# Kernel optimization log

Measured on AMD Instinct MI355X. Metric: run time of the kernel, lower is better.

## Reference

```python
import jax, jax.numpy as jnp
import numpy as np

B, T, E, A = 8, 2048, 1024, 1024


def setup_inputs() -> dict:
    key = jax.random.key(0)
    k1, k2, k3, k4 = jax.random.split(key, 4)
    embedded = jax.random.normal(k1, (B, T, E), dtype=jnp.float32)
    s = 1.0 / np.sqrt(E)
    # nn.Linear(E, A, bias=False) stores weight of shape (A, E); y = x @ W^T
    Wq = jax.random.uniform(k2, (A, E), dtype=jnp.float32, minval=-s, maxval=s)
    Wk = jax.random.uniform(k3, (A, E), dtype=jnp.float32, minval=-s, maxval=s)
    Wv = jax.random.uniform(k4, (A, E), dtype=jnp.float32, minval=-s, maxval=s)
    return {"embedded": embedded, "Wq": Wq, "Wk": Wk, "Wv": Wv}


def reference(embedded, Wq, Wk, Wv):
    # q, k, v: [B, T, A]
    q = jnp.einsum("bte,ae->bta", embedded, Wq)
    k = jnp.einsum("bte,ae->bta", embedded, Wk)
    v = jnp.einsum("bte,ae->bta", embedded, Wv)
    scale = 1.0 / jnp.sqrt(jnp.asarray(Wq.shape[0], dtype=q.dtype))
    # causal scores: [B, T, T]
    scores = jnp.einsum("bqa,bka->bqk", q, k) * scale
    t = scores.shape[-1]
    causal = jnp.tril(jnp.ones((t, t), dtype=bool))
    scores = jnp.where(causal, scores, jnp.asarray(-jnp.inf, dtype=scores.dtype))
    attn = jax.nn.softmax(scores, axis=-1)
    return jnp.einsum("bqk,bka->bqa", attn, v)
```

## Files before the change

### kernel.cpp

```cpp
#include <hip/hip_runtime.h>
#include <hip/hip_bf16.h>
#include <stdint.h>


#define BB 8
#define TT 2048
#define EE 1024
#define AA 1024
#define MM (BB * TT)

typedef short bf16x8 __attribute__((ext_vector_type(8)));
typedef float f32x4 __attribute__((ext_vector_type(4)));

#define GLOAD_LDS16(g, l)                                                      \
  __builtin_amdgcn_global_load_lds(                                            \
      (const __attribute__((address_space(1))) void*)(g),                      \
      (__attribute__((address_space(3))) void*)(l), 16, 0, 0)

#define SBAR()                               \
  do {                                       \
    __builtin_amdgcn_sched_barrier(0);       \
    __builtin_amdgcn_s_barrier();            \
    __builtin_amdgcn_sched_barrier(0);       \
  } while (0)

#define LGKM(n)                                               \
  do {                                                        \
    asm volatile("s_waitcnt lgkmcnt(" #n ")" ::: "memory");   \
    __builtin_amdgcn_sched_barrier(0);                        \
  } while (0)

#define VMCNT(n)                                              \
  do {                                                        \
    asm volatile("s_waitcnt vmcnt(" #n ")" ::: "memory");     \
    __builtin_amdgcn_sched_barrier(0);                        \
  } while (0)

#define MFMA16(a, b, c) __builtin_amdgcn_mfma_f32_16x16x32_bf16((a), (b), (c), 0, 0, 0)

__device__ __forceinline__ void gemm256_core(
    const short* __restrict__ gA, int lda, int a0row,
    const short* __restrict__ gB, int ldb, int b0row, int NT, short* As,
    short* Bs, f32x4 (*acc)[4]) {
  const int tid = threadIdx.x;
  const int lane = tid & 63;
  const int w = tid >> 6;
  const int lrow = lane & 15;
  const int lk8 = (lane >> 4) * 8;
  const int swz = ((lrow >> 3) & 1) << 4;
  const int wr = w >> 2, wc = w & 3;
  const int baseA = (((wr * 128 + lrow) * 32) + lk8) ^ swz;
  const int baseB = (((wc * 64 + lrow) * 32) + lk8) ^ swz;

  const short* pA[2];
  const short* pB[2];
#pragma unroll
  for (int i = 0; i < 2; ++i) {
    int chunk = 2 * w + i;
    int P = chunk * 1024 + lane * 16;
    int L = P ^ (((P >> 9) & 1) << 5);
    int row = L >> 6;
    int kb2 = (L & 63) >> 1;
    pA[i] = gA + (size_t)(a0row + row) * lda + kb2;
    pB[i] = gB + (size_t)(b0row + row) * ldb + kb2;
  }

#define STG_A(tl, s)                                                           \
  do {                                                                         \
    int _o = (tl) * 64 + (s) * 32;                                             \
    short* _d = As + (((tl) & 1) << 14) + ((s) << 13);                         \
    GLOAD_LDS16(pA[0] + _o, _d + (2 * w) * 512 + lane * 8);                    \
    GLOAD_LDS16(pA[1] + _o, _d + (2 * w + 1) * 512 + lane * 8);                \
  } while (0)
#define STG_B(tl, s)                                                           \
  do {                                                                         \
    int _o = (tl) * 64 + (s) * 32;                                             \
    short* _d = Bs + (((tl) & 1) << 14) + ((s) << 13);                         \
    GLOAD_LDS16(pB[0] + _o, _d + (2 * w) * 512 + lane * 8);                    \
    GLOAD_LDS16(pB[1] + _o, _d + (2 * w + 1) * 512 + lane * 8);                \
  } while (0)

  STG_B(0, 0); STG_A(0, 0); STG_B(0, 1); STG_A(0, 1);
  bf16x8 a0[4], b0[4];
  if (NT > 1) {
    STG_B(1, 0); STG_A(1, 0); STG_B(1, 1);
    VMCNT(6);
  } else {
    VMCNT(0);
  }
  SBAR();
#pragma unroll
  for (int m = 0; m < 4; ++m) a0[m] = *(const bf16x8*)&As[baseA + m * 512];
#pragma unroll
  for (int n = 0; n < 4; ++n) b0[n] = *(const bf16x8*)&Bs[baseB + n * 512];

  for (int t = 0; t < NT; ++t) {
    const short* Ac = As + ((t & 1) << 14);
    const short* Bc = Bs + ((t & 1) << 14);
    const short* An = As + (((t + 1) & 1) << 14);
    const short* Bn = Bs + (((t + 1) & 1) << 14);
    bf16x8 a1[4], a2[4], a3[4], b1[4];

    if (t < NT - 1) {
      STG_A(t + 1, 1);
      VMCNT(8);
    } else {
      VMCNT(0);
    }
    SBAR();
#pragma unroll
    for (int m = 0; m < 4; ++m)
      a1[m] = *(const bf16x8*)&Ac[baseA + (m + 4) * 512];
#pragma unroll
    for (int m = 0; m < 4; ++m)
      a2[m] = *(const bf16x8*)&Ac[8192 + baseA + m * 512];
    LGKM(8);
    __builtin_amdgcn_s_setprio(1);
#pragma unroll
    for (int m = 0; m < 4; ++m)
#pragma unroll
      for (int n = 0; n < 4; ++n) acc[m][n] = MFMA16(a0[m], b0[n], acc[m][n]);
    __builtin_amdgcn_s_setprio(0);
    SBAR();

    if (t < NT - 2) STG_B(t + 2, 0);
    SBAR();
#pragma unroll
    for (int n = 0; n < 4; ++n)
      b1[n] = *(const bf16x8*)&Bc[8192 + baseB + n * 512];
    LGKM(4);
    __builtin_amdgcn_s_setprio(1);
#pragma unroll
    for (int m = 0; m < 4; ++m)
#pragma unroll
      for (int n = 0; n < 4; ++n)
        acc[m + 4][n] = MFMA16(a1[m], b0[n], acc[m + 4][n]);
    __builtin_amdgcn_s_setprio(0);
    SBAR();

    if (t < NT - 2) STG_A(t + 2, 0);
    SBAR();
#pragma unroll
    for (int m = 0; m < 4; ++m)
      a3[m] = *(const bf16x8*)&Ac[8192 + baseA + (m + 4) * 512];
    LGKM(4);
    __builtin_amdgcn_s_setprio(1);
#pragma unroll
    for (int m = 0; m < 4; ++m)
#pragma unroll
      for (int n = 0; n < 4; ++n) acc[m][n] = MFMA16(a2[m], b1[n], acc[m][n]);
    __builtin_amdgcn_s_setprio(0);
    SBAR();

    if (t < NT - 2) {
      STG_B(t + 2, 1);
      VMCNT(10);
    } else if (t == NT - 2) {
      VMCNT(4);
    }
    SBAR();
    if (t < NT - 1) {
#pragma unroll
      for (int m = 0; m < 4; ++m) a0[m] = *(const bf16x8*)&An[baseA + m * 512];
#pragma unroll
      for (int n = 0; n < 4; ++n) b0[n] = *(const bf16x8*)&Bn[baseB + n * 512];
      LGKM(8);
    } else {
      LGKM(0);
    }
    __builtin_amdgcn_s_setprio(1);
#pragma unroll
    for (int m = 0; m < 4; ++m)
#pragma unroll
      for (int n = 0; n < 4; ++n)
        acc[m + 4][n] = MFMA16(a3[m], b1[n], acc[m + 4][n]);
    __builtin_amdgcn_s_setprio(0);
    SBAR();
  }
#undef STG_A
#undef STG_B
}

__global__ __launch_bounds__(512, 2) void qkv_gemm8(
    const short* __restrict__ xb, const short* __restrict__ Wb,
    short* __restrict__ qkv) {
  __shared__ __align__(16) short As[32768];
  __shared__ __align__(16) short Bs[32768];
  int f = blockIdx.x;
  int s = (f & 7) * 96 + (f >> 3);
  int mt = s / 12, nt = s % 12;
  int z = nt >> 2, ntl = nt & 3;
  const short* gB = Wb + (size_t)z * AA * EE + (size_t)(ntl * 256) * EE;
  f32x4 acc[8][4];
#pragma unroll
  for (int m = 0; m < 8; ++m)
#pragma unroll
    for (int n = 0; n < 4; ++n) acc[m][n] = (f32x4){0.f, 0.f, 0.f, 0.f};
  gemm256_core(xb, EE, mt * 256, gB, EE, 0, EE / 64, As, Bs, acc);

  short* o = qkv + (size_t)z * MM * AA;
  int lane = threadIdx.x & 63, w = threadIdx.x >> 6, wr = w >> 2, wc = w & 3;
  int lrow = lane & 15, lk4 = (lane >> 4) * 4;
  int row0 = mt * 256 + wr * 128;
  int col0 = ntl * 256 + wc * 64;
#pragma unroll
  for (int m = 0; m < 8; ++m)
#pragma unroll
    for (int n = 0; n < 4; ++n)
#pragma unroll
      for (int r = 0; r < 4; ++r) {
        int row = row0 + m * 16 + lk4 + r;
        int col = col0 + n * 16 + lrow;
        __hip_bfloat16 h = __float2bfloat16(acc[m][n][r]);
        o[(size_t)row * AA + col] = *(short*)&h;
      }
}

__device__ __forceinline__ void stage_tile(const short* __restrict__ g,
                                           size_t stride, short* lds, int tid) {
#pragma unroll
  for (int r = 0; r < 4; ++r) {
    int t = r * 256 + tid;
    int row = t >> 3;
    int c = (t & 7) * 8;
    GLOAD_LDS16(g + (size_t)row * stride + c, lds + (size_t)t * 8);
  }
}

__device__ __forceinline__ void mfma_step(const short* As, const short* Bs,
                                          f32x4 acc[4][4], int lane, int wr,
                                          int wc) {
  int lrow = lane & 15;
  int lk = (lane >> 4) * 8;
#pragma unroll
  for (int kk = 0; kk < 64; kk += 32) {
    bf16x8 a[4], b[4];
#pragma unroll
    for (int i = 0; i < 4; ++i)
      a[i] = *(const bf16x8*)&As[(wr * 64 + i * 16 + lrow) * 64 + kk + lk];
#pragma unroll
    for (int j = 0; j < 4; ++j)
      b[j] = *(const bf16x8*)&Bs[(wc * 64 + j * 16 + lrow) * 64 + kk + lk];
#pragma unroll
    for (int i = 0; i < 4; ++i)
#pragma unroll
      for (int j = 0; j < 4; ++j)
        acc[i][j] =
            __builtin_amdgcn_mfma_f32_16x16x32_bf16(a[i], b[j], acc[i][j], 0, 0, 0);
  }
}

__global__ void cvt_bf16(const float* __restrict__ src, short* __restrict__ dst,
                         int n4) {
  int stride = gridDim.x * blockDim.x;
  for (int i = blockIdx.x * blockDim.x + threadIdx.x; i < n4; i += stride) {
    float4 v = ((const float4*)src)[i];
    __hip_bfloat16 h0 = __float2bfloat16(v.x);
    __hip_bfloat16 h1 = __float2bfloat16(v.y);
    __hip_bfloat16 h2 = __float2bfloat16(v.z);
    __hip_bfloat16 h3 = __float2bfloat16(v.w);
    short4 o;
    o.x = *(short*)&h0;
    o.y = *(short*)&h1;
    o.z = *(short*)&h2;
    o.w = *(short*)&h3;
    ((short4*)dst)[i] = o;
  }
}

__global__ void cvt_w3(const float* __restrict__ wq, const float* __restrict__ wk,
                       const float* __restrict__ wv, short* __restrict__ dst) {
  const int n4 = AA * EE / 4;
  int stride = gridDim.x * blockDim.x;
  for (int i = blockIdx.x * blockDim.x + threadIdx.x; i < 3 * n4; i += stride) {
    const float* src = (i < n4) ? wq : (i < 2 * n4 ? wk : wv);
    int ii = (i < n4) ? i : (i < 2 * n4 ? i - n4 : i - 2 * n4);
    float4 v = ((const float4*)src)[ii];
    __hip_bfloat16 h0 = __float2bfloat16(v.x);
    __hip_bfloat16 h1 = __float2bfloat16(v.y);
    __hip_bfloat16 h2 = __float2bfloat16(v.z);
    __hip_bfloat16 h3 = __float2bfloat16(v.w);
    short4 o;
    o.x = *(short*)&h0;
    o.y = *(short*)&h1;
    o.z = *(short*)&h2;
    o.w = *(short*)&h3;
    ((short4*)dst)[i] = o;
  }
}

__global__ __launch_bounds__(256) void transpose_v(const short* __restrict__ Vb,
                                                   short* __restrict__ Vt) {
  __shared__ __align__(16) short lds[64 * 72];
  int t0 = blockIdx.x * 64;
  int d0 = blockIdx.y * 64;
  int b = blockIdx.z;
  int tid = threadIdx.x;
  const short* src = Vb + ((size_t)b * TT + t0) * AA + d0;
#pragma unroll
  for (int r = 0; r < 2; ++r) {
    int t = r * 256 + tid;
    int row = t >> 3;
    int c = (t & 7) * 8;
    *(bf16x8*)&lds[row * 72 + c] = *(const bf16x8*)&src[(size_t)row * AA + c];
  }
  __syncthreads();
  short* dst = Vt + ((size_t)b * AA + d0) * TT + t0;
#pragma unroll
  for (int r = 0; r < 2; ++r) {
    int t = r * 256 + tid;
    int d = t >> 3;
    int c = (t & 7) * 8;
    bf16x8 wv;
#pragma unroll
    for (int e = 0; e < 8; ++e) wv[e] = lds[(c + e) * 72 + d];
    *(bf16x8*)&dst[(size_t)d * TT + c] = wv;
  }
}

__global__ __launch_bounds__(256) void score_gemm(const short* __restrict__ Qb,
                                                  const short* __restrict__ Kb,
                                                  short* __restrict__ Pu,
                                                  float* __restrict__ lsum) {
  int f = blockIdx.x;
  int b = f & 7;
  int j = f >> 3;
  int mt = 0;
  while ((mt + 1) * (mt + 2) / 2 <= j) ++mt;
  int nt = j - mt * (mt + 1) / 2;
  int q0 = mt * 128, c0 = nt * 128;

  __shared__ __align__(16) short As[128 * 64];
  __shared__ __align__(16) short Bs[128 * 64];
  int tid = threadIdx.x;
  int lane = tid & 63, wid = tid >> 6, wr = wid >> 1, wc = wid & 1;
  const short* Q = Qb + (size_t)b * TT * AA;
  const short* K = Kb + (size_t)b * TT * AA;
  f32x4 acc[4][4];
#pragma unroll
  for (int i = 0; i < 4; ++i)
#pragma unroll
    for (int jj = 0; jj < 4; ++jj) acc[i][jj] = (f32x4){0.f, 0.f, 0.f, 0.f};

  for (int k0 = 0; k0 < AA; k0 += 64) {
    stage_tile(Q + (size_t)q0 * AA + k0, AA, As, tid);
    stage_tile(K + (size_t)c0 * AA + k0, AA, Bs, tid);
    __syncthreads();
    mfma_step(As, Bs, acc, lane, wr, wc);
    __syncthreads();
  }
  const float scale = 0.03125f;
  short* P = Pu + (size_t)b * TT * TT;
  int lrow = lane & 15, lk4 = (lane >> 4) * 4;
#pragma unroll
  for (int i = 0; i < 4; ++i) {
#pragma unroll
    for (int r = 0; r < 4; ++r) {
      int q = q0 + wr * 64 + i * 16 + lk4 + r;
      float rs = 0.f;
#pragma unroll
      for (int jj = 0; jj < 4; ++jj) {
        int kx = c0 + wc * 64 + jj * 16 + lrow;
        float e = (kx <= q) ? __expf(acc[i][jj][r] * scale) : 0.f;
        rs += e;
        __hip_bfloat16 h = __float2bfloat16(e);
        P[(size_t)q * TT + kx] = *(short*)&h;
      }
      rs += __shfl_xor(rs, 1);
      rs += __shfl_xor(rs, 2);
      rs += __shfl_xor(rs, 4);
      rs += __shfl_xor(rs, 8);
      if (lrow == 0) atomicAdd(&lsum[b * TT + q], rs);
    }
  }
}

__global__ __launch_bounds__(256) void pv_gemm(const short* __restrict__ Pu,
                                               const short* __restrict__ Vt,
                                               const float* __restrict__ lsum,
                                               float* __restrict__ out) {
  int f = blockIdx.x;
  int b = f & 7;
  int j = f >> 3;
  int p = j >> 3;
  int nt = j & 7;
  int n0 = nt * 128;

  __shared__ __align__(16) short As[128 * 64];
  __shared__ __align__(16) short Bs[128 * 64];
  int tid = threadIdx.x;
  int lane = tid & 63, wid = tid >> 6, wr = wid >> 1, wc = wid & 1;
  const short* P = Pu + (size_t)b * TT * TT;
  const short* V = Vt + (size_t)b * AA * TT;
  int lrow = lane & 15, lk4 = (lane >> 4) * 4;

#pragma unroll
  for (int s = 0; s < 2; ++s) {
    int mt = s ? (15 - p) : p;
    int q0 = mt * 128;
    f32x4 acc[4][4];
#pragma unroll
    for (int i = 0; i < 4; ++i)
#pragma unroll
      for (int jj = 0; jj < 4; ++jj) acc[i][jj] = (f32x4){0.f, 0.f, 0.f, 0.f};

    int kend = q0 + 128;
    for (int k0 = 0; k0 < kend; k0 += 64) {
      stage_tile(P + (size_t)q0 * TT + k0, TT, As, tid);
      stage_tile(V + (size_t)n0 * TT + k0, TT, Bs, tid);
      __syncthreads();
      mfma_step(As, Bs, acc, lane, wr, wc);
      __syncthreads();
    }
#pragma unroll
    for (int i = 0; i < 4; ++i) {
#pragma unroll
      for (int r = 0; r < 4; ++r) {
        int q = q0 + wr * 64 + i * 16 + lk4 + r;
        float linv = 1.0f / lsum[b * TT + q];
#pragma unroll
        for (int jj = 0; jj < 4; ++jj) {
          int d = n0 + wc * 64 + jj * 16 + lrow;
          out[((size_t)(b * TT + q)) * AA + d] = acc[i][jj][r] * linv;
        }
      }
    }
  }
}

extern "C" void kernel_launch(void* const* d_in, const int* in_sizes, int n_in,
                              void* d_out, int out_size, void* d_ws,
                              size_t ws_size, hipStream_t stream) {
  const float* x = (const float*)d_in[0];
  const float* Wq = (const float*)d_in[1];
  const float* Wk = (const float*)d_in[2];
  const float* Wv = (const float*)d_in[3];

  char* ws = (char*)d_ws;
  size_t oWb = 0;
  size_t oQb = oWb + (size_t)3 * AA * EE * 2;
  size_t oKb = oQb + (size_t)MM * AA * 2;
  size_t oVb = oKb + (size_t)MM * AA * 2;
  size_t oVt = oVb + (size_t)MM * AA * 2;
  size_t oLs = oVt + (size_t)MM * AA * 2;
  size_t oXb = oLs + (size_t)MM * 4;
  size_t oPu = oXb;

  short* Wb = (short*)(ws + oWb);
  short* Qb = (short*)(ws + oQb);
  short* Kb = (short*)(ws + oKb);
  short* Vb = (short*)(ws + oVb);
  short* Vt = (short*)(ws + oVt);
  float* Ls = (float*)(ws + oLs);
  short* Xb = (short*)(ws + oXb);
  short* Pu = (short*)(ws + oPu);

  cvt_bf16<<<2048, 256, 0, stream>>>(x, Xb, MM * EE / 4);
  cvt_w3<<<768, 256, 0, stream>>>(Wq, Wk, Wv, Wb);
  hipMemsetAsync(Ls, 0, (size_t)MM * 4, stream);

  qkv_gemm8<<<768, 512, 0, stream>>>(Xb, Wb, Qb);
  transpose_v<<<dim3(32, 16, 8), 256, 0, stream>>>(Vb, Vt);
  score_gemm<<<1088, 256, 0, stream>>>(Qb, Kb, Pu, Ls);
  pv_gemm<<<512, 256, 0, stream>>>(Pu, Vt, Ls, (float*)d_out);
}
```

Measured before the change: 305.5 us.

## Halve QKV GEMM K-tile and simplify pipeline to raise occupancy

Restructures the QKV projection GEMM main loop from a 64-wide K tile with four interleaved sub-phases to a 32-wide K tile with a simpler two-phase loop. Each iteration loads the A/B fragments, runs two MFMA batches, and prefetches the tile two steps ahead. This halves the LDS footprint and raises the launch-bounds occupancy target from 2 to 4 blocks per CU, aiming to hide latency through more resident waves. The costs are twice as many barriers and global-to-LDS issue rounds per unit of K, and less overlap of LDS reads with MFMAs. The 4-block bound may also force the 128-float accumulator into a tight register budget and cause spills.

```diff
diff --git a/kernel.cpp b/kernel.cpp
--- a/kernel.cpp
+++ b/kernel.cpp
@@ -45,15 +45,16 @@
   const int tid = threadIdx.x;
   const int lane = tid & 63;
   const int w = tid >> 6;
+  const int wr = w >> 2, wc = w & 3;
   const int lrow = lane & 15;
   const int lk8 = (lane >> 4) * 8;
   const int swz = ((lrow >> 3) & 1) << 4;
-  const int wr = w >> 2, wc = w & 3;
   const int baseA = (((wr * 128 + lrow) * 32) + lk8) ^ swz;
   const int baseB = (((wc * 64 + lrow) * 32) + lk8) ^ swz;
 
   const short* pA[2];
   const short* pB[2];
+  int dL[2];
 #pragma unroll
   for (int i = 0; i < 2; ++i) {
     int chunk = 2 * w + i;
@@ -63,129 +64,80 @@
     int kb2 = (L & 63) >> 1;
     pA[i] = gA + (size_t)(a0row + row) * lda + kb2;
     pB[i] = gB + (size_t)(b0row + row) * ldb + kb2;
-  }
-
-#define STG_A(tl, s)                                                           \
+    dL[i] = chunk * 512 + lane * 8;
+  }
+
+#define STG_A(tl)                                                              \
   do {                                                                         \
-    int _o = (tl) * 64 + (s) * 32;                                             \
-    short* _d = As + (((tl) & 1) << 14) + ((s) << 13);                         \
-    GLOAD_LDS16(pA[0] + _o, _d + (2 * w) * 512 + lane * 8);                    \
-    GLOAD_LDS16(pA[1] + _o, _d + (2 * w + 1) * 512 + lane * 8);                \
+    int _o = (tl) * 32;                                                        \
+    short* _d = As + (((tl) & 1) << 13);                                       \
+    GLOAD_LDS16(pA[0] + _o, _d + dL[0]);                                       \
+    GLOAD_LDS16(pA[1] + _o, _d + dL[1]);                                       \
   } while (0)
-#define STG_B(tl, s)                                                           \
+#define STG_B(tl)                                                              \
   do {                                                                         \
-    int _o = (tl) * 64 + (s) * 32;                                             \
-    short* _d = Bs + (((tl) & 1) << 14) + ((s) << 13);                         \
-    GLOAD_LDS16(pB[0] + _o, _d + (2 * w) * 512 + lane * 8);                    \
-    GLOAD_LDS16(pB[1] + _o, _d + (2 * w + 1) * 512 + lane * 8);                \
+    int _o = (tl) * 32;                                                        \
+    short* _d = Bs + (((tl) & 1) << 13);                                       \
+    GLOAD_LDS16(pB[0] + _o, _d + dL[0]);                                       \
+    GLOAD_LDS16(pB[1] + _o, _d + dL[1]);                                       \
   } while (0)
 
-  STG_B(0, 0); STG_A(0, 0); STG_B(0, 1); STG_A(0, 1);
-  bf16x8 a0[4], b0[4];
+  STG_A(0); STG_B(0);
   if (NT > 1) {
-    STG_B(1, 0); STG_A(1, 0); STG_B(1, 1);
-    VMCNT(6);
+    STG_A(1); STG_B(1);
+    VMCNT(4);
   } else {
     VMCNT(0);
   }
   SBAR();
-#pragma unroll
-  for (int m = 0; m < 4; ++m) a0[m] = *(const bf16x8*)&As[baseA + m * 512];
-#pragma unroll
-  for (int n = 0; n < 4; ++n) b0[n] = *(const bf16x8*)&Bs[baseB + n * 512];
 
   for (int t = 0; t < NT; ++t) {
-    const short* Ac = As + ((t & 1) << 14);
-    const short* Bc = Bs + ((t & 1) << 14);
-    const short* An = As + (((t + 1) & 1) << 14);
-    const short* Bn = Bs + (((t + 1) & 1) << 14);
-    bf16x8 a1[4], a2[4], a3[4], b1[4];
-
-    if (t < NT - 1) {
-      STG_A(t + 1, 1);
-      VMCNT(8);
-    } else {
+    const short* Ac = As + ((t & 1) << 13);
+    const short* Bc = Bs + ((t & 1) << 13);
+    bf16x8 a[4], b[4];
+
+#pragma unroll
+    for (int m = 0; m < 4; ++m) a[m] = *(const bf16x8*)&Ac[baseA + m * 512];
+#pragma unroll
+    for (int n = 0; n < 4; ++n) b[n] = *(const bf16x8*)&Bc[baseB + n * 512];
+    LGKM(0);
+    __builtin_amdgcn_s_setprio(1);
+#pragma unroll
+    for (int m = 0; m < 4; ++m)
+#pragma unroll
+      for (int n = 0; n < 4; ++n) acc[m][n] = MFMA16(a[m], b[n], acc[m][n]);
+    __builtin_amdgcn_s_setprio(0);
+
+#pragma unroll
+    for (int m = 0; m < 4; ++m)
+      a[m] = *(const bf16x8*)&Ac[baseA + (m + 4) * 512];
+    LGKM(0);
+    SBAR();
+    if (t < NT - 2) {
+      STG_A(t + 2);
+      STG_B(t + 2);
+      VMCNT(4);
+    } else if (t == NT - 2) {
       VMCNT(0);
     }
     SBAR();
+    __builtin_amdgcn_s_setprio(1);
 #pragma unroll
     for (int m = 0; m < 4; ++m)
-      a1[m] = *(const bf16x8*)&Ac[baseA + (m + 4) * 512];
-#pragma unroll
-    for (int m = 0; m < 4; ++m)
-      a2[m] = *(const bf16x8*)&Ac[8192 + baseA + m * 512];
-    LGKM(8);
-    __builtin_amdgcn_s_setprio(1);
-#pragma unroll
-    for (int m = 0; m < 4; ++m)
-#pragma unroll
-      for (int n = 0; n < 4; ++n) acc[m][n] = MFMA16(a0[m], b0[n], acc[m][n]);
+#pragma unroll
+      for (int n = 0; n < 4; ++n)
+        acc[m + 4][n] = MFMA16(a[m], b[n], acc[m + 4][n]);
     __builtin_amdgcn_s_setprio(0);
-    SBAR();
-
-    if (t < NT - 2) STG_B(t + 2, 0);
-    SBAR();
-#pragma unroll
-    for (int n = 0; n < 4; ++n)
-      b1[n] = *(const bf16x8*)&Bc[8192 + baseB + n * 512];
-    LGKM(4);
-    __builtin_amdgcn_s_setprio(1);
-#pragma unroll
-    for (int m = 0; m < 4; ++m)
-#pragma unroll
-      for (int n = 0; n < 4; ++n)
-        acc[m + 4][n] = MFMA16(a1[m], b0[n], acc[m + 4][n]);
-    __builtin_amdgcn_s_setprio(0);
-    SBAR();
-
-    if (t < NT - 2) STG_A(t + 2, 0);
-    SBAR();
-#pragma unroll
-    for (int m = 0; m < 4; ++m)
-      a3[m] = *(const bf16x8*)&Ac[8192 + baseA + (m + 4) * 512];
-    LGKM(4);
-    __builtin_amdgcn_s_setprio(1);
-#pragma unroll
-    for (int m = 0; m < 4; ++m)
-#pragma unroll
-      for (int n = 0; n < 4; ++n) acc[m][n] = MFMA16(a2[m], b1[n], acc[m][n]);
-    __builtin_amdgcn_s_setprio(0);
-    SBAR();
-
-    if (t < NT - 2) {
-      STG_B(t + 2, 1);
-      VMCNT(10);
-    } else if (t == NT - 2) {
-      VMCNT(4);
-    }
-    SBAR();
-    if (t < NT - 1) {
-#pragma unroll
-      for (int m = 0; m < 4; ++m) a0[m] = *(const bf16x8*)&An[baseA + m * 512];
-#pragma unroll
-      for (int n = 0; n < 4; ++n) b0[n] = *(const bf16x8*)&Bn[baseB + n * 512];
-      LGKM(8);
-    } else {
-      LGKM(0);
-    }
-    __builtin_amdgcn_s_setprio(1);
-#pragma unroll
-    for (int m = 0; m < 4; ++m)
-#pragma unroll
-      for (int n = 0; n < 4; ++n)
-        acc[m + 4][n] = MFMA16(a3[m], b1[n], acc[m + 4][n]);
-    __builtin_amdgcn_s_setprio(0);
-    SBAR();
   }
 #undef STG_A
 #undef STG_B
 }
 
-__global__ __launch_bounds__(512, 2) void qkv_gemm8(
+__global__ __launch_bounds__(512, 4) void qkv_gemm8(
     const short* __restrict__ xb, const short* __restrict__ Wb,
     short* __restrict__ qkv) {
-  __shared__ __align__(16) short As[32768];
-  __shared__ __align__(16) short Bs[32768];
+  __shared__ __align__(16) short As[16384];
+  __shared__ __align__(16) short Bs[16384];
   int f = blockIdx.x;
   int s = (f & 7) * 96 + (f >> 3);
   int mt = s / 12, nt = s % 12;
@@ -196,7 +148,7 @@
   for (int m = 0; m < 8; ++m)
 #pragma unroll
     for (int n = 0; n < 4; ++n) acc[m][n] = (f32x4){0.f, 0.f, 0.f, 0.f};
-  gemm256_core(xb, EE, mt * 256, gB, EE, 0, EE / 64, As, Bs, acc);
+  gemm256_core(xb, EE, mt * 256, gB, EE, 0, EE / 32, As, Bs, acc);
 
   short* o = qkv + (size_t)z * MM * AA;
   int lane = threadIdx.x & 63, w = threadIdx.x >> 6, wr = w >> 2, wc = w & 3;
```

Result: slower. 1.017 ms (+233.0%).
